# Kernel optimization log

Hardware: AMD Instinct MI355X
Metric: run time of the kernel (lower is better)

The kernel has to match this reference:

```python
import jax, jax.numpy as jnp
import numpy as np

DEPTH, HEADS, DIM, DIM_HEAD, MLP = 2, 8, 512, 64, 2048
INNER = HEADS * DIM_HEAD  # == DIM here, but project_out is still True since dim_head != dim
NEG = -1e9


def _ln(t, g, b):
    mu = t.mean(-1, keepdims=True)
    var = ((t - mu) ** 2).mean(-1, keepdims=True)
    return (t - mu) / jnp.sqrt(var + 1e-5) * g + b


def _heads(t):
    b, n, hd = t.shape
    return t.reshape(b, n, HEADS, hd // HEADS).transpose(0, 2, 1, 3)  # b h n d


def _merge(t):
    b, h, n, d = t.shape
    return t.transpose(0, 2, 1, 3).reshape(b, n, h * d)


def kat_forward(x, kx, rd, clst, mask, kmask,
                ln1_g, ln1_b, Wqkv, Wout, bout, ln2_g, ln2_b, W1, b1, W2, b2):
    scale = DIM_HEAD ** -0.5
    # att_mask[b,1,n,m]: True where attention is disallowed (mask_i * kmask_j < 0.5)
    att_mask = (jnp.einsum('bid,bjd->bij', mask, kmask) < 0.5)[:, None]
    krd = rd[:, None]                      # [b,1,m,n]
    krdT = jnp.swapaxes(krd, -1, -2)       # [b,1,n,m]
    keep = (kmask >= 0.5)                  # kernel_mask fill-with-0 complement
    k_reps, atten = [], []
    for l in range(DEPTH):
        # pre-norm applied in-place before residual (as in the original)
        xn = _ln(x, ln1_g[l], ln1_b[l])
        kxn = _ln(kx, ln1_g[l], ln1_b[l])
        cn = _ln(clst, ln1_g[l], ln1_b[l])

        def qkv(t):
            q, k, v = jnp.split(t @ Wqkv[l], 3, axis=-1)
            return _heads(q), _heads(k), _heads(v)

        tq, tk, tv = qkv(xn)
        kq, kk, kv = qkv(kxn)
        cq, _, _ = qkv(cn)

        # patch -> kernel attention, krd-weighted dual softmax
        dots = jnp.einsum('bhid,bhjd->bhij', tq, kk) * scale      # [b,h,n,m]
        dots = jnp.where(att_mask, NEG, dots)
        attn_t = jax.nn.softmax(dots * 24, -1) * krdT             # temperature branch (attention map out)
        attn = jax.nn.softmax(dots, -1) * krdT
        x_ = _merge(jnp.einsum('bhij,bhjd->bhid', attn, kv)) @ Wout[l] + bout[l]

        # kernel -> patch attention
        kd = jnp.einsum('bhid,bhjd->bhij', kq, tk) * scale        # [b,h,m,n]
        kd = jnp.where(jnp.swapaxes(att_mask, -1, -2), NEG, kd)
        kattn = jax.nn.softmax(kd, -1) * krd
        kx_ = _merge(jnp.einsum('bhij,bhjd->bhid', kattn, tv)) @ Wout[l] + bout[l]

        # class token -> kernel attention
        cd = jnp.einsum('bhid,bhjd->bhij', cq, kk) * scale        # [b,h,1,m]
        cd = jnp.where(att_mask[:, :, :1], NEG, cd)
        c_ = _merge(jnp.einsum('bhij,bhjd->bhid', jax.nn.softmax(cd, -1), kv)) @ Wout[l] + bout[l]

        x, kx, clst = xn + x_, kxn + kx_, cn + c_

        def ff(t):
            tn = _ln(t, ln2_g[l], ln2_b[l])
            return jax.nn.gelu(tn @ W1[l] + b1[l], approximate=False) @ W2[l] + b2[l]

        x, kx, clst = ff(x) + x, ff(kx) + kx, ff(clst) + clst
        k_reps.append(kx * keep)
        atten.append(jnp.swapaxes(attn_t, -1, -2))  # [b,h,m,n]
    return jnp.stack(k_reps), clst, jnp.stack(atten)


def setup_inputs() -> dict:
    key = jax.random.key(0)
    ks = jax.random.split(key, 16)
    b, n, m = 4, 2048, 256
    s = 0.02
    L = DEPTH
    return {
        'x': jax.random.normal(ks[0], (b, n, DIM), jnp.float32),
        'kx': jax.random.normal(ks[1], (b, m, DIM), jnp.float32),
        'rd': jax.random.uniform(ks[2], (b, m, n), jnp.float32),
        'clst': jax.random.normal(ks[3], (b, 1, DIM), jnp.float32),
        'mask': jnp.ones((b, n, 1), jnp.float32),
        'kmask': jax.random.uniform(ks[4], (b, m, 1), jnp.float32),
        'ln1_g': jnp.ones((L, DIM), jnp.float32),
        'ln1_b': jnp.zeros((L, DIM), jnp.float32),
        'Wqkv': s * jax.random.normal(ks[5], (L, DIM, 3 * INNER), jnp.float32),
        'Wout': s * jax.random.normal(ks[6], (L, INNER, DIM), jnp.float32),
        'bout': jnp.zeros((L, DIM), jnp.float32),
        'ln2_g': jnp.ones((L, DIM), jnp.float32),
        'ln2_b': jnp.zeros((L, DIM), jnp.float32),
        'W1': s * jax.random.normal(ks[7], (L, DIM, MLP), jnp.float32),
        'b1': jnp.zeros((L, MLP), jnp.float32),
        'W2': s * jax.random.normal(ks[8], (L, MLP, DIM), jnp.float32),
        'b2': jnp.zeros((L, DIM), jnp.float32),
    }


def reference(x, kx, rd, clst, mask, kmask, ln1_g, ln1_b, Wqkv, Wout, bout,
              ln2_g, ln2_b, W1, b1, W2, b2):
    return kat_forward(x, kx, rd, clst, mask, kmask, ln1_g, ln1_b, Wqkv, Wout,
                       bout, ln2_g, ln2_b, W1, b1, W2, b2)
```

## Files before the change

### kernel.cpp

```cpp
#include <hip/hip_runtime.h>
#include <hip/hip_bf16.h>
#include <cstddef>

#define DEV __device__ __forceinline__

constexpr int Bb  = 4;
constexpr int Nn  = 2048;
constexpr int MK  = 256;
constexpr int Dd  = 512;
constexpr int Hh  = 8;
constexpr int DH  = 64;
constexpr int QLD = 1536;
constexpr int MLPD = 2048;
constexpr int NTOK = Bb * Nn + Bb * MK + Bb;
constexpr int KXOFF = Bb * Nn;
constexpr int CLOFF = Bb * Nn + Bb * MK;
constexpr float SCALE = 0.125f;
constexpr float NEGV  = -1e9f;

typedef __attribute__((ext_vector_type(8))) short short8;
typedef __attribute__((ext_vector_type(4))) float f32x4;

DEV float4 ldf4(const float* p) { return *reinterpret_cast<const float4*>(p); }

DEV void gload16(const short* g, short* l) {
  __builtin_amdgcn_global_load_lds(
      (const __attribute__((address_space(1))) void*)g,
      (__attribute__((address_space(3))) void*)l, 16, 0, 0);
}

DEV float waveMax(float v) {
#pragma unroll
  for (int o = 32; o; o >>= 1) v = fmaxf(v, __shfl_xor(v, o));
  return v;
}
DEV float waveSum(float v) {
#pragma unroll
  for (int o = 32; o; o >>= 1) v += __shfl_xor(v, o);
  return v;
}
DEV float blockMax256(float v, float* red) {
  v = waveMax(v);
  __syncthreads();
  if ((threadIdx.x & 63) == 0) red[threadIdx.x >> 6] = v;
  __syncthreads();
  return fmaxf(fmaxf(red[0], red[1]), fmaxf(red[2], red[3]));
}
DEV float blockSum256(float v, float* red) {
  v = waveSum(v);
  __syncthreads();
  if ((threadIdx.x & 63) == 0) red[threadIdx.x >> 6] = v;
  __syncthreads();
  return red[0] + red[1] + red[2] + red[3];
}
DEV float gelu_f(float x) { return 0.5f * x * (1.f + erff(x * 0.70710678118654752f)); }
DEV float pow24(float e1) {
  float e2 = e1 * e1, e4 = e2 * e2, e8 = e4 * e4, e16 = e8 * e8;
  return e16 * e8;
}

__global__ __launch_bounds__(256)
void copy3_kernel(const float* __restrict__ x, const float* __restrict__ kx,
                  const float* __restrict__ c, float* __restrict__ dst) {
  const int idx = blockIdx.x * 256 + threadIdx.x;
  const int row = idx >> 7;
  float4 v;
  if (row < KXOFF) v = ldf4(x + (size_t)idx * 4);
  else if (row < CLOFF) v = ldf4(kx + (size_t)idx * 4 - (size_t)KXOFF * Dd);
  else v = ldf4(c + (size_t)idx * 4 - (size_t)CLOFF * Dd);
  *reinterpret_cast<float4*>(dst + (size_t)idx * 4) = v;
}

__global__ __launch_bounds__(64)
void ln_kernel(const float* __restrict__ in, const float* __restrict__ gw,
               const float* __restrict__ bw, float* __restrict__ out,
               __hip_bfloat16* __restrict__ outb) {
  const int row = blockIdx.x;
  const int t = threadIdx.x;
  const float* p = in + (size_t)row * Dd + t * 8;
  float4 v0 = ldf4(p), v1 = ldf4(p + 4);
  float s = v0.x + v0.y + v0.z + v0.w + v1.x + v1.y + v1.z + v1.w;
  float q = v0.x*v0.x + v0.y*v0.y + v0.z*v0.z + v0.w*v0.w
          + v1.x*v1.x + v1.y*v1.y + v1.z*v1.z + v1.w*v1.w;
  s = waveSum(s); q = waveSum(q);
  const float mu = s * (1.f / Dd);
  const float rstd = rsqrtf(fmaxf(q * (1.f / Dd) - mu * mu, 0.f) + 1e-5f);
  float4 g0 = ldf4(gw + t * 8), g1 = ldf4(gw + t * 8 + 4);
  float4 b0 = ldf4(bw + t * 8), b1 = ldf4(bw + t * 8 + 4);
  float o[8];
  o[0] = (v0.x - mu) * rstd * g0.x + b0.x;
  o[1] = (v0.y - mu) * rstd * g0.y + b0.y;
  o[2] = (v0.z - mu) * rstd * g0.z + b0.z;
  o[3] = (v0.w - mu) * rstd * g0.w + b0.w;
  o[4] = (v1.x - mu) * rstd * g1.x + b1.x;
  o[5] = (v1.y - mu) * rstd * g1.y + b1.y;
  o[6] = (v1.z - mu) * rstd * g1.z + b1.z;
  o[7] = (v1.w - mu) * rstd * g1.w + b1.w;
  float* op = out + (size_t)row * Dd + t * 8;
  *reinterpret_cast<float4*>(op)     = make_float4(o[0], o[1], o[2], o[3]);
  *reinterpret_cast<float4*>(op + 4) = make_float4(o[4], o[5], o[6], o[7]);
  __hip_bfloat16* ob = outb + (size_t)row * Dd + t * 8;
#pragma unroll
  for (int e = 0; e < 8; ++e) ob[e] = __float2bfloat16(o[e]);
}

struct GArgs {
  const short* A;  long asb; int lda;
  const short* Bt; long bsb; int ldb;
  float* C; __hip_bfloat16* Cb;
  long czo, czi; int ldc;
  const float* bias;
  const float* res; int ldr;
  int M, N, K;
};

template<int BM, int BN, int EPI>
__global__ __launch_bounds__(256)
void mgemm(GArgs g) {
  constexpr int WMW = (BN >= 128) ? 2 : 4;
  constexpr int WNW = 4 / WMW;
  constexpr int WM = BM / WMW, WN = BN / WNW;
  constexpr int FM = WM / 16, FN = WN / 16;
  __shared__ __align__(16) short As[BM * 64];
  __shared__ __align__(16) short Bs[BN * 64];
  const int tid = threadIdx.x, l = tid & 63, w = tid >> 6;
  const int wm = (WNW == 2) ? (w >> 1) : w;
  const int wn = (WNW == 2) ? (w & 1) : 0;
  int bx = blockIdx.x, by = blockIdx.y;
  {
    const int gx = gridDim.x, nwg = gx * gridDim.y;
    const int orig = by * gx + bx;
    const int xcd = orig & 7, pos = orig >> 3;
    const int q = nwg >> 3, rmd = nwg & 7;
    const int s = (xcd < rmd ? xcd * (q + 1) : rmd * (q + 1) + (xcd - rmd) * q) + pos;
    bx = s % gx; by = s / gx;
  }
  const int z = blockIdx.z;
  const short* Ab = g.A + (size_t)z * g.asb;
  const short* Bb_ = g.Bt + (size_t)z * g.bsb;
  f32x4 acc[FM][FN] = {};
  const int lr = l & 15, lg = l >> 4;

  for (int k0 = 0; k0 < g.K; k0 += 64) {
    __syncthreads();
#pragma unroll
    for (int it = 0; it < BM / 32; ++it) {
      int idx = tid + it * 256, r = idx >> 3, c = idx & 7;
      int gm = by * BM + r;
      if (gm >= g.M) gm = g.M - 1;
      gload16(Ab + (size_t)gm * g.lda + k0 + ((c ^ (r & 7)) * 8), As + idx * 8);
    }
#pragma unroll
    for (int it = 0; it < BN / 32; ++it) {
      int idx = tid + it * 256, r = idx >> 3, c = idx & 7;
      int gn = bx * BN + r;
      gload16(Bb_ + (size_t)gn * g.ldb + k0 + ((c ^ (r & 7)) * 8), Bs + idx * 8);
    }
    __syncthreads();
#pragma unroll
    for (int ks = 0; ks < 2; ++ks) {
      short8 a[FM], b[FN];
#pragma unroll
      for (int fm = 0; fm < FM; ++fm) {
        int rr = wm * WM + fm * 16 + lr;
        int ch = (ks * 4 + lg) ^ (rr & 7);
        a[fm] = *reinterpret_cast<const short8*>(As + rr * 64 + ch * 8);
      }
#pragma unroll
      for (int fn = 0; fn < FN; ++fn) {
        int rn = wn * WN + fn * 16 + lr;
        int ch = (ks * 4 + lg) ^ (rn & 7);
        b[fn] = *reinterpret_cast<const short8*>(Bs + rn * 64 + ch * 8);
      }
#pragma unroll
      for (int fm = 0; fm < FM; ++fm)
#pragma unroll
        for (int fn = 0; fn < FN; ++fn)
          acc[fm][fn] = __builtin_amdgcn_mfma_f32_16x16x32_bf16(a[fm], b[fn], acc[fm][fn], 0, 0, 0);
    }
  }

  const size_t zoff = (size_t)(z >> 3) * g.czo + (size_t)(z & 7) * g.czi;
#pragma unroll
  for (int fm = 0; fm < FM; ++fm) {
#pragma unroll
    for (int fn = 0; fn < FN; ++fn) {
#pragma unroll
      for (int r = 0; r < 4; ++r) {
        int m = by * BM + wm * WM + fm * 16 + lg * 4 + r;
        int n = bx * BN + wn * WN + fn * 16 + lr;
        if (m >= g.M) continue;
        float v = acc[fm][fn][r];
        size_t coff = zoff + (size_t)m * g.ldc + n;
        if (EPI == 0) {
          g.C[coff] = v;
        } else if (EPI == 2) {
          v += g.bias[n] + g.res[(size_t)m * g.ldr + n];
          g.C[coff] = v;
        } else if (EPI == 3) {
          v = gelu_f(v + g.bias[n]);
          g.Cb[coff] = __float2bfloat16(v);
        } else {
          g.Cb[coff] = __float2bfloat16(v);
        }
      }
    }
  }
}

template<int BM, int BN, int EPI>
static void launch_mgemm(const GArgs& g, int zdim, hipStream_t s) {
  dim3 grid((g.N + BN - 1) / BN, (g.M + BM - 1) / BM, zdim);
  mgemm<BM, BN, EPI><<<grid, 256, 0, s>>>(g);
}

__global__ __launch_bounds__(512)
void score_sx_kernel(const short* __restrict__ Q, const short* __restrict__ Km,
                     const float* __restrict__ mask, const float* __restrict__ kmask,
                     const float* __restrict__ rdT,
                     __hip_bfloat16* __restrict__ P1, __hip_bfloat16* __restrict__ E24) {
  __shared__ __align__(16) short As[128 * 64];
  __shared__ __align__(16) short Bs[256 * 64];
  __shared__ float red[128 * 2];
  __shared__ float red2[128 * 4];
  const int tid = threadIdx.x, l = tid & 63, w = tid >> 6;
  const int wm = w >> 1, wn = w & 1;
  const int by = blockIdx.x, bh = blockIdx.y;
  const int b = bh >> 3;
  const short* Ab = Q + (size_t)bh * Nn * 128;
  const short* Bb = Km + (size_t)bh * MK * 128;
  const int lr = l & 15, lg = l >> 4;
  f32x4 acc[2][8] = {};

  for (int k0 = 0; k0 < 128; k0 += 64) {
    __syncthreads();
#pragma unroll
    for (int it = 0; it < 2; ++it) {
      int idx = tid + it * 512, r = idx >> 3, c = idx & 7;
      gload16(Ab + (size_t)(by * 128 + r) * 128 + k0 + ((c ^ (r & 7)) * 8), As + idx * 8);
    }
#pragma unroll
    for (int it = 0; it < 4; ++it) {
      int idx = tid + it * 512, r = idx >> 3, c = idx & 7;
      gload16(Bb + (size_t)r * 128 + k0 + ((c ^ (r & 7)) * 8), Bs + idx * 8);
    }
    __syncthreads();
#pragma unroll
    for (int ks = 0; ks < 2; ++ks) {
      short8 a[2], bv[8];
#pragma unroll
      for (int fm = 0; fm < 2; ++fm) {
        int rr = wm * 32 + fm * 16 + lr;
        int ch = (ks * 4 + lg) ^ (rr & 7);
        a[fm] = *reinterpret_cast<const short8*>(As + rr * 64 + ch * 8);
      }
#pragma unroll
      for (int fn = 0; fn < 8; ++fn) {
        int rn = wn * 128 + fn * 16 + lr;
        int ch = (ks * 4 + lg) ^ (rn & 7);
        bv[fn] = *reinterpret_cast<const short8*>(Bs + rn * 64 + ch * 8);
      }
#pragma unroll
      for (int fm = 0; fm < 2; ++fm)
#pragma unroll
        for (int fn = 0; fn < 8; ++fn)
          acc[fm][fn] = __builtin_amdgcn_mfma_f32_16x16x32_bf16(a[fm], bv[fn], acc[fm][fn], 0, 0, 0);
    }
  }
  {
    float colm[8];
#pragma unroll
    for (int fn = 0; fn < 8; ++fn)
      colm[fn] = kmask[b * MK + wn * 128 + fn * 16 + lr];
#pragma unroll
    for (int fm = 0; fm < 2; ++fm)
#pragma unroll
      for (int r = 0; r < 4; ++r) {
        float rm = mask[(size_t)b * Nn + by * 128 + wm * 32 + fm * 16 + lg * 4 + r];
#pragma unroll
        for (int fn = 0; fn < 8; ++fn)
          acc[fm][fn][r] = (rm * colm[fn] < 0.5f) ? NEGV : acc[fm][fn][r] * SCALE;
      }
  }
  float mx[2][4];
#pragma unroll
  for (int fm = 0; fm < 2; ++fm)
#pragma unroll
    for (int r = 0; r < 4; ++r) {
      float m = -3.4e38f;
#pragma unroll
      for (int fn = 0; fn < 8; ++fn) m = fmaxf(m, acc[fm][fn][r]);
#pragma unroll
      for (int o = 8; o; o >>= 1) m = fmaxf(m, __shfl_xor(m, o));
      mx[fm][r] = m;
    }
  __syncthreads();
  if (lr == 0) {
#pragma unroll
    for (int fm = 0; fm < 2; ++fm)
#pragma unroll
      for (int r = 0; r < 4; ++r)
        red[(wm * 32 + fm * 16 + lg * 4 + r) * 2 + wn] = mx[fm][r];
  }
  __syncthreads();
#pragma unroll
  for (int fm = 0; fm < 2; ++fm)
#pragma unroll
    for (int r = 0; r < 4; ++r) {
      int row = wm * 32 + fm * 16 + lg * 4 + r;
      mx[fm][r] = fmaxf(red[row * 2], red[row * 2 + 1]);
    }
  float s1[2][4], s24[2][4];
#pragma unroll
  for (int fm = 0; fm < 2; ++fm)
#pragma unroll
    for (int r = 0; r < 4; ++r) {
      float a1 = 0.f, a24 = 0.f;
#pragma unroll
      for (int fn = 0; fn < 8; ++fn) {
        float e1 = __expf(acc[fm][fn][r] - mx[fm][r]);
        acc[fm][fn][r] = e1;
        a1 += e1;
        a24 += pow24(e1);
      }
#pragma unroll
      for (int o = 8; o; o >>= 1) { a1 += __shfl_xor(a1, o); a24 += __shfl_xor(a24, o); }
      s1[fm][r] = a1; s24[fm][r] = a24;
    }
  __syncthreads();
  if (lr == 0) {
#pragma unroll
    for (int fm = 0; fm < 2; ++fm)
#pragma unroll
      for (int r = 0; r < 4; ++r) {
        int row = wm * 32 + fm * 16 + lg * 4 + r;
        red2[row * 4 + wn * 2]     = s1[fm][r];
        red2[row * 4 + wn * 2 + 1] = s24[fm][r];
      }
  }
  __syncthreads();
#pragma unroll
  for (int fm = 0; fm < 2; ++fm)
#pragma unroll
    for (int r = 0; r < 4; ++r) {
      int row = wm * 32 + fm * 16 + lg * 4 + r;
      s1[fm][r]  = 1.f / (red2[row * 4] + red2[row * 4 + 2]);
      s24[fm][r] = 1.f / (red2[row * 4 + 1] + red2[row * 4 + 3]);
    }
#pragma unroll
  for (int fm = 0; fm < 2; ++fm) {
#pragma unroll
    for (int r = 0; r < 4; ++r) {
      int m = by * 128 + wm * 32 + fm * 16 + lg * 4 + r;
      const float* rp = rdT + ((size_t)b * Nn + m) * MK;
      size_t obase = ((size_t)bh * Nn + m) * MK;
#pragma unroll
      for (int fn = 0; fn < 8; ++fn) {
        int n = wn * 128 + fn * 16 + lr;
        float e1 = acc[fm][fn][r];
        float rv = rp[n];
        P1[obase + n]  = __float2bfloat16(e1 * s1[fm][r] * rv);
        E24[obase + n] = __float2bfloat16(pow24(e1) * s24[fm][r] * rv);
      }
    }
  }
}

__global__ __launch_bounds__(256)
void score_sk_kernel(const short* __restrict__ Qk, const short* __restrict__ Kt,
                     const float* __restrict__ mask, const float* __restrict__ kmask,
                     const float* __restrict__ rd, __hip_bfloat16* __restrict__ P2) {
  __shared__ __align__(16) short As[16 * 64];
  __shared__ __align__(16) short Bs[256 * 64];
  __shared__ float redm[16 * 4];
  __shared__ float reds[16 * 4];
  const int tid = threadIdx.x, l = tid & 63, w = tid >> 6;
  const int lr = l & 15, lg = l >> 4;
  const int bh = blockIdx.x, j0 = blockIdx.y * 16, b = bh >> 3;
  const short* Ab = Qk + ((size_t)bh * MK + j0) * 64;
  const short* Bb = Kt + (size_t)bh * Nn * 64;
  f32x4 acc[32];
#pragma unroll
  for (int q = 0; q < 32; ++q) acc[q] = f32x4{0.f, 0.f, 0.f, 0.f};
  if (tid < 128) {
    int r = tid >> 3, c = tid & 7;
    gload16(Ab + (size_t)r * 64 + ((c ^ (r & 7)) * 8), As + tid * 8);
  }
#pragma unroll
  for (int nc = 0; nc < 8; ++nc) {
    __syncthreads();
#pragma unroll
    for (int it = 0; it < 8; ++it) {
      int idx = tid + it * 256, r = idx >> 3, c = idx & 7;
      gload16(Bb + (size_t)(nc * 256 + r) * 64 + ((c ^ (r & 7)) * 8), Bs + idx * 8);
    }
    __syncthreads();
#pragma unroll
    for (int ks = 0; ks < 2; ++ks) {
      short8 a;
      {
        int ch = (ks * 4 + lg) ^ (lr & 7);
        a = *reinterpret_cast<const short8*>(As + lr * 64 + ch * 8);
      }
#pragma unroll
      for (int fn = 0; fn < 4; ++fn) {
        int rn = w * 64 + fn * 16 + lr;
        int ch = (ks * 4 + lg) ^ (rn & 7);
        short8 bv = *reinterpret_cast<const short8*>(Bs + rn * 64 + ch * 8);
        acc[nc * 4 + fn] =
            __builtin_amdgcn_mfma_f32_16x16x32_bf16(a, bv, acc[nc * 4 + fn], 0, 0, 0);
      }
    }
  }
  float rm[4];
#pragma unroll
  for (int rr = 0; rr < 4; ++rr) rm[rr] = kmask[b * MK + j0 + lg * 4 + rr];
  float mx[4] = {-3.4e38f, -3.4e38f, -3.4e38f, -3.4e38f};
#pragma unroll
  for (int q = 0; q < 32; ++q) {
    int n = (q >> 2) * 256 + w * 64 + (q & 3) * 16 + lr;
    float cm = mask[(size_t)b * Nn + n];
#pragma unroll
    for (int rr = 0; rr < 4; ++rr) {
      float v = (rm[rr] * cm < 0.5f) ? NEGV : acc[q][rr] * SCALE;
      acc[q][rr] = v;
      mx[rr] = fmaxf(mx[rr], v);
    }
  }
#pragma unroll
  for (int o = 8; o; o >>= 1)
#pragma unroll
    for (int rr = 0; rr < 4; ++rr) mx[rr] = fmaxf(mx[rr], __shfl_xor(mx[rr], o));
  __syncthreads();
  if (lr == 0) {
#pragma unroll
    for (int rr = 0; rr < 4; ++rr) redm[(lg * 4 + rr) * 4 + w] = mx[rr];
  }
  __syncthreads();
#pragma unroll
  for (int rr = 0; rr < 4; ++rr) {
    int row = lg * 4 + rr;
    mx[rr] = fmaxf(fmaxf(redm[row * 4], redm[row * 4 + 1]),
                   fmaxf(redm[row * 4 + 2], redm[row * 4 + 3]));
  }
  float sm[4] = {0.f, 0.f, 0.f, 0.f};
#pragma unroll
  for (int q = 0; q < 32; ++q)
#pragma unroll
    for (int rr = 0; rr < 4; ++rr) {
      float e = __expf(acc[q][rr] - mx[rr]);
      acc[q][rr] = e;
      sm[rr] += e;
    }
#pragma unroll
  for (int o = 8; o; o >>= 1)
#pragma unroll
    for (int rr = 0; rr < 4; ++rr) sm[rr] += __shfl_xor(sm[rr], o);
  __syncthreads();
  if (lr == 0) {
#pragma unroll
    for (int rr = 0; rr < 4; ++rr) reds[(lg * 4 + rr) * 4 + w] = sm[rr];
  }
  __syncthreads();
  float inv[4];
#pragma unroll
  for (int rr = 0; rr < 4; ++rr) {
    int row = lg * 4 + rr;
    inv[rr] = 1.f / (reds[row * 4] + reds[row * 4 + 1] + reds[row * 4 + 2] + reds[row * 4 + 3]);
  }
#pragma unroll
  for (int rr = 0; rr < 4; ++rr) {
    int j = j0 + lg * 4 + rr;
    const float* rp = rd + (size_t)(b * MK + j) * Nn;
    __hip_bfloat16* pp = P2 + ((size_t)bh * MK + j) * Nn;
#pragma unroll
    for (int q = 0; q < 32; ++q) {
      int n = (q >> 2) * 256 + w * 64 + (q & 3) * 16 + lr;
      pp[n] = __float2bfloat16(acc[q][rr] * inv[rr] * rp[n]);
    }
  }
}

__global__ __launch_bounds__(256)
void at_tr_kernel(const __hip_bfloat16* __restrict__ E, float* __restrict__ atten) {
  __shared__ __hip_bfloat16 t[64][72];
  const int bh = blockIdx.x;
  const int i0 = blockIdx.y * 64, j0 = blockIdx.z * 64;
  const int tid = threadIdx.x;
#pragma unroll
  for (int it = 0; it < 2; ++it) {
    int idx = tid + it * 256, r = idx >> 3, c8 = (idx & 7) * 8;
    short8 v = *reinterpret_cast<const short8*>(
        (const short*)E + ((size_t)bh * Nn + i0 + r) * MK + j0 + c8);
#pragma unroll
    for (int e = 0; e < 8; ++e)
      *reinterpret_cast<short*>(&t[r][c8 + e]) = v[e];
  }
  __syncthreads();
#pragma unroll
  for (int it = 0; it < 4; ++it) {
    int idx = tid + it * 256, jr = idx >> 4, c4 = (idx & 15) * 4;
    float4 o;
    o.x = __bfloat162float(t[c4 + 0][jr]);
    o.y = __bfloat162float(t[c4 + 1][jr]);
    o.z = __bfloat162float(t[c4 + 2][jr]);
    o.w = __bfloat162float(t[c4 + 3][jr]);
    *reinterpret_cast<float4*>(
        atten + ((size_t)bh * MK + j0 + jr) * Nn + i0 + c4) = o;
  }
}

__global__ __launch_bounds__(256)
void rd_tr_kernel(const float* __restrict__ rd, float* __restrict__ rdT) {
  __shared__ float tb[64][65];
  const int b = blockIdx.x;
  const int i0 = blockIdx.y * 64, j0 = blockIdx.z * 64;
  const int tid = threadIdx.x;
#pragma unroll
  for (int it = 0; it < 4; ++it) {
    int idx = tid + it * 256, r = idx >> 4, c4 = (idx & 15) * 4;
    float4 v = ldf4(rd + ((size_t)(b * MK + j0 + r)) * Nn + i0 + c4);
    tb[r][c4 + 0] = v.x; tb[r][c4 + 1] = v.y; tb[r][c4 + 2] = v.z; tb[r][c4 + 3] = v.w;
  }
  __syncthreads();
#pragma unroll
  for (int it = 0; it < 4; ++it) {
    int idx = tid + it * 256, r = idx >> 4, c4 = (idx & 15) * 4;
    float4 o = make_float4(tb[c4 + 0][r], tb[c4 + 1][r], tb[c4 + 2][r], tb[c4 + 3][r]);
    *reinterpret_cast<float4*>(rdT + ((size_t)(b * Nn + i0 + r)) * MK + j0 + c4) = o;
  }
}

struct WtArgs {
  const float* W[8];
  __hip_bfloat16* T[8];
  int K[8], N[8];
};
__global__ __launch_bounds__(256)
void wtrans_all_kernel(WtArgs a) {
  __shared__ float t[64][65];
  const int e = blockIdx.z;
  const int K = a.K[e], N = a.N[e];
  const int n0 = blockIdx.x * 64, k0 = blockIdx.y * 64;
  if (n0 >= N || k0 >= K) return;
  const float* W = a.W[e];
  __hip_bfloat16* WT = a.T[e];
  const int tid = threadIdx.x;
#pragma unroll
  for (int it = 0; it < 4; ++it) {
    int idx = tid + it * 256, r = idx >> 4, f = idx & 15;
    float4 v = ldf4(W + (size_t)(k0 + r) * N + n0 + f * 4);
    t[r][f * 4 + 0] = v.x; t[r][f * 4 + 1] = v.y;
    t[r][f * 4 + 2] = v.z; t[r][f * 4 + 3] = v.w;
  }
  __syncthreads();
#pragma unroll
  for (int it = 0; it < 4; ++it) {
    int idx = tid + it * 256, r = idx >> 4, c4 = (idx & 15) * 4;
    __hip_bfloat16* op = WT + (size_t)(n0 + r) * K + k0 + c4;
#pragma unroll
    for (int e2 = 0; e2 < 4; ++e2) op[e2] = __float2bfloat16(t[c4 + e2][r]);
  }
}

template<bool Q_SPLIT>
__global__ __launch_bounds__(256)
void split_kernel(const float* __restrict__ qkv, __hip_bfloat16* __restrict__ qout,
                  __hip_bfloat16* __restrict__ kout, int T) {
  const int idx = blockIdx.x * 256 + threadIdx.x;
  const int token = idx >> 7, c8 = (idx & 127) * 8;
  const int b = token / T, i = token - b * T;
  const float* p = qkv + (size_t)token * QLD + c8;
  float v[8];
  float4 a = ldf4(p), c = ldf4(p + 4);
  v[0]=a.x; v[1]=a.y; v[2]=a.z; v[3]=a.w; v[4]=c.x; v[5]=c.y; v[6]=c.z; v[7]=c.w;
  if (c8 < 512) {
    int h = c8 >> 6, d = c8 & 63;
    if (Q_SPLIT) {
      __hip_bfloat16* q = qout + ((size_t)((b * 8 + h) * T + i)) * 128 + d;
#pragma unroll
      for (int e = 0; e < 8; ++e) {
        __hip_bfloat16 hi = __float2bfloat16(v[e]);
        q[e] = hi;
        q[64 + e] = __float2bfloat16(v[e] - __bfloat162float(hi));
      }
    } else {
      __hip_bfloat16* q = qout + ((size_t)((b * 8 + h) * T + i)) * 64 + d;
#pragma unroll
      for (int e = 0; e < 8; ++e) q[e] = __float2bfloat16(v[e]);
    }
  } else {
    int cc = c8 - 512, h = cc >> 6, d = cc & 63;
    if (Q_SPLIT) {
      __hip_bfloat16* k = kout + ((size_t)((b * 8 + h) * T + i)) * 64 + d;
#pragma unroll
      for (int e = 0; e < 8; ++e) k[e] = __float2bfloat16(v[e]);
    } else {
      __hip_bfloat16* k = kout + ((size_t)((b * 8 + h) * T + i)) * 128 + d;
#pragma unroll
      for (int e = 0; e < 8; ++e) {
        __hip_bfloat16 hi = __float2bfloat16(v[e]);
        k[e] = hi;
        k[64 + e] = __float2bfloat16(v[e] - __bfloat162float(hi));
      }
    }
  }
}

__global__ __launch_bounds__(256)
void vtrans_kernel(const float* __restrict__ qkv, __hip_bfloat16* __restrict__ vT, int T) {
  __shared__ float t[64][65];
  const int bh = blockIdx.x, b = bh >> 3, h = bh & 7;
  const int i0 = blockIdx.y * 64;
  const int tid = threadIdx.x;
#pragma unroll
  for (int it = 0; it < 4; ++it) {
    int idx = tid + it * 256, r = idx >> 4, f = idx & 15;
    float4 v = ldf4(qkv + (size_t)(b * T + i0 + r) * QLD + 2 * Dd + h * 64 + f * 4);
    t[r][f * 4 + 0] = v.x; t[r][f * 4 + 1] = v.y;
    t[r][f * 4 + 2] = v.z; t[r][f * 4 + 3] = v.w;
  }
  __syncthreads();
#pragma unroll
  for (int it = 0; it < 4; ++it) {
    int idx = tid + it * 256, d = idx >> 4, c4 = (idx & 15) * 4;
    __hip_bfloat16* op = vT + (size_t)(bh * 64 + d) * T + i0 + c4;
#pragma unroll
    for (int e = 0; e < 4; ++e) op[e] = __float2bfloat16(t[c4 + e][d]);
  }
}

__global__ __launch_bounds__(256)
void attn_c_kernel(const float* __restrict__ cqkv, const float* __restrict__ kqkv,
                   const float* __restrict__ mask, const float* __restrict__ kmask,
                   __hip_bfloat16* __restrict__ c_pre) {
  __shared__ __align__(16) float kv_s[MK][DH];
  __shared__ __align__(16) float q_s[DH];
  __shared__ float pbuf[MK];
  __shared__ float red8[8];
  __shared__ float redpv[4][DH];
  const int tid = threadIdx.x;
  const int bh = blockIdx.x, b = bh >> 3, h = bh & 7;
  const float* vp = kqkv + ((size_t)(b * MK + tid)) * QLD + 2 * Dd + h * DH;
#pragma unroll
  for (int q4 = 0; q4 < 16; ++q4)
    *reinterpret_cast<float4*>(&kv_s[tid][q4 * 4]) = ldf4(vp + q4 * 4);
  if (tid < DH) q_s[tid] = cqkv[(size_t)b * QLD + h * DH + tid];
  __syncthreads();
  const float* kp = kqkv + ((size_t)(b * MK + tid)) * QLD + Dd + h * DH;
  float dot = 0.f;
#pragma unroll
  for (int q4 = 0; q4 < 16; ++q4) {
    float4 kv4 = ldf4(kp + q4 * 4);
    float4 qv = ldf4(&q_s[q4 * 4]);
    dot = fmaf(qv.x, kv4.x, dot);
    dot = fmaf(qv.y, kv4.y, dot);
    dot = fmaf(qv.z, kv4.z, dot);
    dot = fmaf(qv.w, kv4.w, dot);
  }
  const float dm = (mask[(size_t)b * Nn] * kmask[b * MK + tid] < 0.5f) ? NEGV : dot * SCALE;
  const float mx = blockMax256(dm, red8);
  const float e = __expf(dm - mx);
  const float s = blockSum256(e, red8);
  pbuf[tid] = e / s;
  __syncthreads();
  const int d = tid & 63, g = tid >> 6;
  float acc = 0.f;
#pragma unroll 8
  for (int jj = 0; jj < 64; ++jj)
    acc = fmaf(pbuf[g * 64 + jj], kv_s[g * 64 + jj][d], acc);
  redpv[g][d] = acc;
  __syncthreads();
  if (tid < DH)
    c_pre[(size_t)b * Dd + h * DH + tid] = __float2bfloat16(
        redpv[0][tid] + redpv[1][tid] + redpv[2][tid] + redpv[3][tid]);
}

__global__ void kreps_kernel(const float* __restrict__ kx, const float* __restrict__ kmask,
                             float* __restrict__ o) {
  const int idx = blockIdx.x * 256 + threadIdx.x;
  const int bj = idx >> 9;
  const float keep = (kmask[bj] >= 0.5f) ? 1.f : 0.f;
  o[idx] = kx[idx] * keep;
}
__global__ void cout_kernel(const float* __restrict__ c_s, float* __restrict__ o) {
  const int idx = blockIdx.x * 256 + threadIdx.x;
  o[idx] = c_s[idx];
}

static GArgs ga_base() { GArgs g = {}; return g; }

extern "C" void kernel_launch(void* const* d_in, const int* in_sizes, int n_in,
                              void* d_out, int out_size, void* d_ws, size_t ws_size,
                              hipStream_t stream) {
  (void)in_sizes; (void)n_in; (void)out_size; (void)ws_size;
  const float* x_in  = (const float*)d_in[0];
  const float* kx_in = (const float*)d_in[1];
  const float* rd    = (const float*)d_in[2];
  const float* c_in  = (const float*)d_in[3];
  const float* mask  = (const float*)d_in[4];
  const float* kmask = (const float*)d_in[5];
  const float* ln1g  = (const float*)d_in[6];
  const float* ln1b  = (const float*)d_in[7];
  const float* Wqkv  = (const float*)d_in[8];
  const float* Woutw = (const float*)d_in[9];
  const float* boutw = (const float*)d_in[10];
  const float* ln2g  = (const float*)d_in[11];
  const float* ln2b  = (const float*)d_in[12];
  const float* W1    = (const float*)d_in[13];
  const float* b1    = (const float*)d_in[14];
  const float* W2    = (const float*)d_in[15];
  const float* b2    = (const float*)d_in[16];
  float* out = (float*)d_out;

  float* ws = (float*)d_ws;
  size_t off = 0;
  auto alloc = [&](size_t n) { float* p = ws + off; off += (n + 15) & ~(size_t)15; return p; };
  float* xcat_s    = alloc((size_t)NTOK * Dd);
  float* xcat_n    = alloc((size_t)NTOK * Dd);
  float* xcat_nb_f = alloc((size_t)NTOK * Dd / 2);
  float* pre_cat_f = alloc((size_t)NTOK * Dd / 2);
  float* qkv       = alloc((size_t)NTOK * QLD);
  float* P1_f      = alloc((size_t)32 * Nn * MK / 2);
  float* E24_f     = alloc((size_t)32 * Nn * MK / 2);
  float* P2_f      = alloc((size_t)32 * MK * Nn / 2);
  float* tq_s_f    = alloc((size_t)32 * Nn * 128 / 2);
  float* kk_s_f    = alloc((size_t)32 * MK * 128 / 2);
  float* tk_hi_f   = alloc((size_t)32 * Nn * 64 / 2);
  float* kq_hi_f   = alloc((size_t)32 * MK * 64 / 2);
  float* tvT_f     = alloc((size_t)32 * 64 * Nn / 2);
  float* kvT_f     = alloc((size_t)32 * 64 * MK / 2);
  float* rdT       = alloc((size_t)Bb * Nn * MK);
  float* WqkvT_f   = alloc((size_t)2 * QLD * Dd / 2);
  float* WoutT_f   = alloc((size_t)2 * Dd * Dd / 2);
  float* W1T_f     = alloc((size_t)2 * MLPD * Dd / 2);
  float* W2T_f     = alloc((size_t)2 * Dd * MLPD / 2);

  __hip_bfloat16* xcat_nb = (__hip_bfloat16*)xcat_nb_f;
  __hip_bfloat16* pre_cat = (__hip_bfloat16*)pre_cat_f;
  __hip_bfloat16* P1b     = (__hip_bfloat16*)P1_f;
  __hip_bfloat16* E24b    = (__hip_bfloat16*)E24_f;
  __hip_bfloat16* P2b     = (__hip_bfloat16*)P2_f;
  __hip_bfloat16* tq_s    = (__hip_bfloat16*)tq_s_f;
  __hip_bfloat16* kk_s    = (__hip_bfloat16*)kk_s_f;
  __hip_bfloat16* tk_hi   = (__hip_bfloat16*)tk_hi_f;
  __hip_bfloat16* kq_hi   = (__hip_bfloat16*)kq_hi_f;
  __hip_bfloat16* tvT     = (__hip_bfloat16*)tvT_f;
  __hip_bfloat16* kvT     = (__hip_bfloat16*)kvT_f;
  __hip_bfloat16* WqkvT   = (__hip_bfloat16*)WqkvT_f;
  __hip_bfloat16* WoutT   = (__hip_bfloat16*)WoutT_f;
  __hip_bfloat16* W1T     = (__hip_bfloat16*)W1T_f;
  __hip_bfloat16* W2T     = (__hip_bfloat16*)W2T_f;
  __hip_bfloat16* hid     = (__hip_bfloat16*)qkv;

  const size_t CL_OFF = (size_t)2 * Bb * MK * Dd;
  const size_t AT_OFF = CL_OFF + (size_t)Bb * Dd;

  copy3_kernel<<<(NTOK * 128) / 256, 256, 0, stream>>>(x_in, kx_in, c_in, xcat_s);
  rd_tr_kernel<<<dim3(Bb, Nn / 64, MK / 64), 256, 0, stream>>>(rd, rdT);
  {
    WtArgs a;
    for (int l = 0; l < 2; ++l) {
      a.W[l * 4 + 0] = Wqkv + (size_t)l * Dd * QLD;  a.T[l * 4 + 0] = WqkvT + (size_t)l * QLD * Dd;
      a.K[l * 4 + 0] = Dd;   a.N[l * 4 + 0] = QLD;
      a.W[l * 4 + 1] = Woutw + (size_t)l * Dd * Dd;  a.T[l * 4 + 1] = WoutT + (size_t)l * Dd * Dd;
      a.K[l * 4 + 1] = Dd;   a.N[l * 4 + 1] = Dd;
      a.W[l * 4 + 2] = W1 + (size_t)l * Dd * MLPD;   a.T[l * 4 + 2] = W1T + (size_t)l * MLPD * Dd;
      a.K[l * 4 + 2] = Dd;   a.N[l * 4 + 2] = MLPD;
      a.W[l * 4 + 3] = W2 + (size_t)l * MLPD * Dd;   a.T[l * 4 + 3] = W2T + (size_t)l * Dd * MLPD;
      a.K[l * 4 + 3] = MLPD; a.N[l * 4 + 3] = Dd;
    }
    wtrans_all_kernel<<<dim3(32, 32, 8), 256, 0, stream>>>(a);
  }

  for (int l = 0; l < 2; ++l) {
    const float* bo  = boutw + (size_t)l * Dd;
    const float* b1l = b1 + (size_t)l * MLPD;
    const float* b2l = b2 + (size_t)l * Dd;
    __hip_bfloat16* WqkvTl = WqkvT + (size_t)l * QLD * Dd;
    __hip_bfloat16* WoutTl = WoutT + (size_t)l * Dd * Dd;
    __hip_bfloat16* W1Tl   = W1T + (size_t)l * MLPD * Dd;
    __hip_bfloat16* W2Tl   = W2T + (size_t)l * Dd * MLPD;

    ln_kernel<<<NTOK, 64, 0, stream>>>(xcat_s, ln1g + l * Dd, ln1b + l * Dd, xcat_n, xcat_nb);

    {
      GArgs g = ga_base();
      g.A = (const short*)xcat_nb; g.lda = Dd;
      g.Bt = (const short*)WqkvTl; g.ldb = Dd;
      g.C = qkv; g.ldc = QLD;
      g.M = NTOK; g.N = QLD; g.K = Dd;
      launch_mgemm<128, 128, 0>(g, 1, stream);
    }

    split_kernel<true><<<(Bb * Nn * 128) / 256, 256, 0, stream>>>(qkv, tq_s, tk_hi, Nn);
    split_kernel<false><<<(Bb * MK * 128) / 256, 256, 0, stream>>>(
        qkv + (size_t)KXOFF * QLD, kq_hi, kk_s, MK);
    vtrans_kernel<<<dim3(32, Nn / 64), 256, 0, stream>>>(qkv, tvT, Nn);
    vtrans_kernel<<<dim3(32, MK / 64), 256, 0, stream>>>(qkv + (size_t)KXOFF * QLD, kvT, MK);

    attn_c_kernel<<<Bb * Hh, 256, 0, stream>>>(qkv + (size_t)CLOFF * QLD,
                                               qkv + (size_t)KXOFF * QLD, mask, kmask,
                                               pre_cat + (size_t)CLOFF * Dd);

    score_sx_kernel<<<dim3(Nn / 128, 32), 512, 0, stream>>>(
        (const short*)tq_s, (const short*)kk_s, mask, kmask, rdT, P1b, E24b);
    at_tr_kernel<<<dim3(32, Nn / 64, MK / 64), 256, 0, stream>>>(
        E24b, out + AT_OFF + (size_t)l * 32 * MK * Nn);
    {
      GArgs g = ga_base();
      g.A = (const short*)P1b; g.asb = (long)Nn * MK; g.lda = MK;
      g.Bt = (const short*)kvT; g.bsb = (long)64 * MK; g.ldb = MK;
      g.Cb = pre_cat; g.czo = (long)Nn * Dd; g.czi = 64; g.ldc = Dd;
      g.M = Nn; g.N = 64; g.K = MK;
      launch_mgemm<128, 64, 4>(g, 32, stream);
    }
    score_sk_kernel<<<dim3(32, MK / 16), 256, 0, stream>>>(
        (const short*)kq_hi, (const short*)tk_hi, mask, kmask, rd, P2b);
    {
      GArgs g = ga_base();
      g.A = (const short*)P2b; g.asb = (long)MK * Nn; g.lda = Nn;
      g.Bt = (const short*)tvT; g.bsb = (long)64 * Nn; g.ldb = Nn;
      g.Cb = pre_cat + (size_t)KXOFF * Dd; g.czo = (long)MK * Dd; g.czi = 64; g.ldc = Dd;
      g.M = MK; g.N = 64; g.K = Nn;
      launch_mgemm<64, 64, 4>(g, 32, stream);
    }

    {
      GArgs g = ga_base();
      g.A = (const short*)pre_cat; g.lda = Dd;
      g.Bt = (const short*)WoutTl; g.ldb = Dd;
      g.C = xcat_s; g.ldc = Dd; g.bias = bo; g.res = xcat_n; g.ldr = Dd;
      g.M = NTOK; g.N = Dd; g.K = Dd;
      launch_mgemm<128, 64, 2>(g, 1, stream);
    }

    ln_kernel<<<NTOK, 64, 0, stream>>>(xcat_s, ln2g + l * Dd, ln2b + l * Dd, xcat_n, xcat_nb);
    {
      GArgs g = ga_base();
      g.A = (const short*)xcat_nb; g.lda = Dd;
      g.Bt = (const short*)W1Tl; g.ldb = Dd;
      g.Cb = hid; g.ldc = MLPD; g.bias = b1l;
      g.M = NTOK; g.N = MLPD; g.K = Dd;
      launch_mgemm<128, 128, 3>(g, 1, stream);
      GArgs h = ga_base();
      h.A = (const short*)hid; h.lda = MLPD;
      h.Bt = (const short*)W2Tl; h.ldb = MLPD;
      h.C = xcat_s; h.ldc = Dd; h.bias = b2l; h.res = xcat_s; h.ldr = Dd;
      h.M = NTOK; h.N = Dd; h.K = MLPD;
      launch_mgemm<128, 64, 2>(h, 1, stream);
    }

    kreps_kernel<<<(Bb * MK * Dd) / 256, 256, 0, stream>>>(
        xcat_s + (size_t)KXOFF * Dd, kmask, out + (size_t)l * Bb * MK * Dd);
  }
  cout_kernel<<<(Bb * Dd) / 256, 256, 0, stream>>>(xcat_s + (size_t)CLOFF * Dd, out + CL_OFF);
}
```

Measured before the change: 772.3 us.

## Fuse QKV split/transpose kernels, drop fp32 LN output, loop at_tr over j

Merges the two split kernels and two V-transpose kernels into one prep_attn launch. LayerNorm no longer writes an fp32 copy; the out-projection residual now reads the bf16 normalized activations via a new epilogue. at_tr_kernel processes all four j-tiles per block instead of one block per tile. The aim is fewer launches and less fp32 memory traffic, at the cost of lower residual precision (bf16 instead of fp32) and fewer, larger transpose blocks.

```diff
diff --git a/kernel.cpp b/kernel.cpp
--- a/kernel.cpp
+++ b/kernel.cpp
@@ -73,8 +73,7 @@
 
 __global__ __launch_bounds__(64)
 void ln_kernel(const float* __restrict__ in, const float* __restrict__ gw,
-               const float* __restrict__ bw, float* __restrict__ out,
-               __hip_bfloat16* __restrict__ outb) {
+               const float* __restrict__ bw, __hip_bfloat16* __restrict__ outb) {
   const int row = blockIdx.x;
   const int t = threadIdx.x;
   const float* p = in + (size_t)row * Dd + t * 8;
@@ -96,9 +95,6 @@
   o[5] = (v1.y - mu) * rstd * g1.y + b1.y;
   o[6] = (v1.z - mu) * rstd * g1.z + b1.z;
   o[7] = (v1.w - mu) * rstd * g1.w + b1.w;
-  float* op = out + (size_t)row * Dd + t * 8;
-  *reinterpret_cast<float4*>(op)     = make_float4(o[0], o[1], o[2], o[3]);
-  *reinterpret_cast<float4*>(op + 4) = make_float4(o[4], o[5], o[6], o[7]);
   __hip_bfloat16* ob = outb + (size_t)row * Dd + t * 8;
 #pragma unroll
   for (int e = 0; e < 8; ++e) ob[e] = __float2bfloat16(o[e]);
@@ -110,7 +106,7 @@
   float* C; __hip_bfloat16* Cb;
   long czo, czi; int ldc;
   const float* bias;
-  const float* res; int ldr;
+  const float* res; const __hip_bfloat16* resb; int ldr;
   int M, N, K;
 };
 
@@ -197,6 +193,9 @@
         } else if (EPI == 2) {
           v += g.bias[n] + g.res[(size_t)m * g.ldr + n];
           g.C[coff] = v;
+        } else if (EPI == 5) {
+          v += g.bias[n] + __bfloat162float(g.resb[(size_t)m * g.ldr + n]);
+          g.C[coff] = v;
         } else if (EPI == 3) {
           v = gelu_f(v + g.bias[n]);
           g.Cb[coff] = __float2bfloat16(v);
@@ -212,6 +211,82 @@
 static void launch_mgemm(const GArgs& g, int zdim, hipStream_t s) {
   dim3 grid((g.N + BN - 1) / BN, (g.M + BM - 1) / BM, zdim);
   mgemm<BM, BN, EPI><<<grid, 256, 0, s>>>(g);
+}
+
+__global__ __launch_bounds__(256)
+void prep_attn_kernel(const float* __restrict__ qkv_x, const float* __restrict__ qkv_k,
+                      __hip_bfloat16* __restrict__ tq_s, __hip_bfloat16* __restrict__ tk_hi,
+                      __hip_bfloat16* __restrict__ kq_hi, __hip_bfloat16* __restrict__ kk_s,
+                      __hip_bfloat16* __restrict__ tvT, __hip_bfloat16* __restrict__ kvT) {
+  __shared__ float t[64][65];
+  const int blk = blockIdx.x, tid = threadIdx.x;
+  if (blk < 4096 + 512) {
+    const bool isX = blk < 4096;
+    const int T = isX ? Nn : MK;
+    const float* qkv = isX ? qkv_x : qkv_k;
+    const int idx = (isX ? blk : blk - 4096) * 256 + tid;
+    const int token = idx >> 7, c8 = (idx & 127) * 8;
+    const int b = token / T, i = token - b * T;
+    const float* p = qkv + (size_t)token * QLD + c8;
+    float v[8];
+    float4 a = ldf4(p), c = ldf4(p + 4);
+    v[0]=a.x; v[1]=a.y; v[2]=a.z; v[3]=a.w; v[4]=c.x; v[5]=c.y; v[6]=c.z; v[7]=c.w;
+    if (c8 < 512) {
+      int h = c8 >> 6, d = c8 & 63;
+      if (isX) {
+        __hip_bfloat16* q = tq_s + ((size_t)((b * 8 + h) * T + i)) * 128 + d;
+#pragma unroll
+        for (int e = 0; e < 8; ++e) {
+          __hip_bfloat16 hi = __float2bfloat16(v[e]);
+          q[e] = hi;
+          q[64 + e] = __float2bfloat16(v[e] - __bfloat162float(hi));
+        }
+      } else {
+        __hip_bfloat16* q = kq_hi + ((size_t)((b * 8 + h) * T + i)) * 64 + d;
+#pragma unroll
+        for (int e = 0; e < 8; ++e) q[e] = __float2bfloat16(v[e]);
+      }
+    } else {
+      int cc = c8 - 512, h = cc >> 6, d = cc & 63;
+      if (isX) {
+        __hip_bfloat16* k = tk_hi + ((size_t)((b * 8 + h) * T + i)) * 64 + d;
+#pragma unroll
+        for (int e = 0; e < 8; ++e) k[e] = __float2bfloat16(v[e]);
+      } else {
+        __hip_bfloat16* k = kk_s + ((size_t)((b * 8 + h) * T + i)) * 128 + d;
+#pragma unroll
+        for (int e = 0; e < 8; ++e) {
+          __hip_bfloat16 hi = __float2bfloat16(v[e]);
+          k[e] = hi;
+          k[64 + e] = __float2bfloat16(v[e] - __bfloat162float(hi));
+        }
+      }
+    }
+    return;
+  }
+  const bool isX = blk < 5632;
+  const int r = isX ? blk - 4608 : blk - 5632;
+  const int T = isX ? Nn : MK;
+  const int tilesPerBh = T / 64;
+  const int bh = r / tilesPerBh, i0 = (r % tilesPerBh) * 64;
+  const int b = bh >> 3, h = bh & 7;
+  const float* qkv = isX ? qkv_x : qkv_k;
+  __hip_bfloat16* vT = isX ? tvT : kvT;
+#pragma unroll
+  for (int it = 0; it < 4; ++it) {
+    int idx = tid + it * 256, rr = idx >> 4, f = idx & 15;
+    float4 v = ldf4(qkv + (size_t)(b * T + i0 + rr) * QLD + 2 * Dd + h * 64 + f * 4);
+    t[rr][f * 4 + 0] = v.x; t[rr][f * 4 + 1] = v.y;
+    t[rr][f * 4 + 2] = v.z; t[rr][f * 4 + 3] = v.w;
+  }
+  __syncthreads();
+#pragma unroll
+  for (int it = 0; it < 4; ++it) {
+    int idx = tid + it * 256, d = idx >> 4, c4 = (idx & 15) * 4;
+    __hip_bfloat16* op = vT + (size_t)(bh * 64 + d) * T + i0 + c4;
+#pragma unroll
+    for (int e = 0; e < 4; ++e) op[e] = __float2bfloat16(t[c4 + e][d]);
+  }
 }
 
 __global__ __launch_bounds__(512)
@@ -485,28 +560,32 @@
 void at_tr_kernel(const __hip_bfloat16* __restrict__ E, float* __restrict__ atten) {
   __shared__ __hip_bfloat16 t[64][72];
   const int bh = blockIdx.x;
-  const int i0 = blockIdx.y * 64, j0 = blockIdx.z * 64;
+  const int i0 = blockIdx.y * 64;
   const int tid = threadIdx.x;
-#pragma unroll
-  for (int it = 0; it < 2; ++it) {
-    int idx = tid + it * 256, r = idx >> 3, c8 = (idx & 7) * 8;
-    short8 v = *reinterpret_cast<const short8*>(
-        (const short*)E + ((size_t)bh * Nn + i0 + r) * MK + j0 + c8);
-#pragma unroll
-    for (int e = 0; e < 8; ++e)
-      *reinterpret_cast<short*>(&t[r][c8 + e]) = v[e];
-  }
-  __syncthreads();
-#pragma unroll
-  for (int it = 0; it < 4; ++it) {
-    int idx = tid + it * 256, jr = idx >> 4, c4 = (idx & 15) * 4;
-    float4 o;
-    o.x = __bfloat162float(t[c4 + 0][jr]);
-    o.y = __bfloat162float(t[c4 + 1][jr]);
-    o.z = __bfloat162float(t[c4 + 2][jr]);
-    o.w = __bfloat162float(t[c4 + 3][jr]);
-    *reinterpret_cast<float4*>(
-        atten + ((size_t)bh * MK + j0 + jr) * Nn + i0 + c4) = o;
+  for (int jt = 0; jt < 4; ++jt) {
+    const int j0 = jt * 64;
+    if (jt) __syncthreads();
+#pragma unroll
+    for (int it = 0; it < 2; ++it) {
+      int idx = tid + it * 256, r = idx >> 3, c8 = (idx & 7) * 8;
+      short8 v = *reinterpret_cast<const short8*>(
+          (const short*)E + ((size_t)bh * Nn + i0 + r) * MK + j0 + c8);
+#pragma unroll
+      for (int e = 0; e < 8; ++e)
+        *reinterpret_cast<short*>(&t[r][c8 + e]) = v[e];
+    }
+    __syncthreads();
+#pragma unroll
+    for (int it = 0; it < 4; ++it) {
+      int idx = tid + it * 256, jr = idx >> 4, c4 = (idx & 15) * 4;
+      float4 o;
+      o.x = __bfloat162float(t[c4 + 0][jr]);
+      o.y = __bfloat162float(t[c4 + 1][jr]);
+      o.z = __bfloat162float(t[c4 + 2][jr]);
+      o.w = __bfloat162float(t[c4 + 3][jr]);
+      *reinterpret_cast<float4*>(
+          atten + ((size_t)bh * MK + j0 + jr) * Nn + i0 + c4) = o;
+    }
   }
 }
 
@@ -560,73 +639,6 @@
     __hip_bfloat16* op = WT + (size_t)(n0 + r) * K + k0 + c4;
 #pragma unroll
     for (int e2 = 0; e2 < 4; ++e2) op[e2] = __float2bfloat16(t[c4 + e2][r]);
-  }
-}
-
-template<bool Q_SPLIT>
-__global__ __launch_bounds__(256)
-void split_kernel(const float* __restrict__ qkv, __hip_bfloat16* __restrict__ qout,
-                  __hip_bfloat16* __restrict__ kout, int T) {
-  const int idx = blockIdx.x * 256 + threadIdx.x;
-  const int token = idx >> 7, c8 = (idx & 127) * 8;
-  const int b = token / T, i = token - b * T;
-  const float* p = qkv + (size_t)token * QLD + c8;
-  float v[8];
-  float4 a = ldf4(p), c = ldf4(p + 4);
-  v[0]=a.x; v[1]=a.y; v[2]=a.z; v[3]=a.w; v[4]=c.x; v[5]=c.y; v[6]=c.z; v[7]=c.w;
-  if (c8 < 512) {
-    int h = c8 >> 6, d = c8 & 63;
-    if (Q_SPLIT) {
-      __hip_bfloat16* q = qout + ((size_t)((b * 8 + h) * T + i)) * 128 + d;
-#pragma unroll
-      for (int e = 0; e < 8; ++e) {
-        __hip_bfloat16 hi = __float2bfloat16(v[e]);
-        q[e] = hi;
-        q[64 + e] = __float2bfloat16(v[e] - __bfloat162float(hi));
-      }
-    } else {
-      __hip_bfloat16* q = qout + ((size_t)((b * 8 + h) * T + i)) * 64 + d;
-#pragma unroll
-      for (int e = 0; e < 8; ++e) q[e] = __float2bfloat16(v[e]);
-    }
-  } else {
-    int cc = c8 - 512, h = cc >> 6, d = cc & 63;
-    if (Q_SPLIT) {
-      __hip_bfloat16* k = kout + ((size_t)((b * 8 + h) * T + i)) * 64 + d;
-#pragma unroll
-      for (int e = 0; e < 8; ++e) k[e] = __float2bfloat16(v[e]);
-    } else {
-      __hip_bfloat16* k = kout + ((size_t)((b * 8 + h) * T + i)) * 128 + d;
-#pragma unroll
-      for (int e = 0; e < 8; ++e) {
-        __hip_bfloat16 hi = __float2bfloat16(v[e]);
-        k[e] = hi;
-        k[64 + e] = __float2bfloat16(v[e] - __bfloat162float(hi));
-      }
-    }
-  }
-}
-
-__global__ __launch_bounds__(256)
-void vtrans_kernel(const float* __restrict__ qkv, __hip_bfloat16* __restrict__ vT, int T) {
-  __shared__ float t[64][65];
-  const int bh = blockIdx.x, b = bh >> 3, h = bh & 7;
-  const int i0 = blockIdx.y * 64;
-  const int tid = threadIdx.x;
-#pragma unroll
-  for (int it = 0; it < 4; ++it) {
-    int idx = tid + it * 256, r = idx >> 4, f = idx & 15;
-    float4 v = ldf4(qkv + (size_t)(b * T + i0 + r) * QLD + 2 * Dd + h * 64 + f * 4);
-    t[r][f * 4 + 0] = v.x; t[r][f * 4 + 1] = v.y;
-    t[r][f * 4 + 2] = v.z; t[r][f * 4 + 3] = v.w;
-  }
-  __syncthreads();
-#pragma unroll
-  for (int it = 0; it < 4; ++it) {
-    int idx = tid + it * 256, d = idx >> 4, c4 = (idx & 15) * 4;
-    __hip_bfloat16* op = vT + (size_t)(bh * 64 + d) * T + i0 + c4;
-#pragma unroll
-    for (int e = 0; e < 4; ++e) op[e] = __float2bfloat16(t[c4 + e][d]);
   }
 }
 
@@ -717,7 +729,6 @@
   size_t off = 0;
   auto alloc = [&](size_t n) { float* p = ws + off; off += (n + 15) & ~(size_t)15; return p; };
   float* xcat_s    = alloc((size_t)NTOK * Dd);
-  float* xcat_n    = alloc((size_t)NTOK * Dd);
   float* xcat_nb_f = alloc((size_t)NTOK * Dd / 2);
   float* pre_cat_f = alloc((size_t)NTOK * Dd / 2);
   float* qkv       = alloc((size_t)NTOK * QLD);
@@ -782,7 +793,7 @@
     __hip_bfloat16* W1Tl   = W1T + (size_t)l * MLPD * Dd;
     __hip_bfloat16* W2Tl   = W2T + (size_t)l * Dd * MLPD;
 
-    ln_kernel<<<NTOK, 64, 0, stream>>>(xcat_s, ln1g + l * Dd, ln1b + l * Dd, xcat_n, xcat_nb);
+    ln_kernel<<<NTOK, 64, 0, stream>>>(xcat_s, ln1g + l * Dd, ln1b + l * Dd, xcat_nb);
 
     {
       GArgs g = ga_base();
@@ -793,11 +804,8 @@
       launch_mgemm<128, 128, 0>(g, 1, stream);
     }
 
-    split_kernel<true><<<(Bb * Nn * 128) / 256, 256, 0, stream>>>(qkv, tq_s, tk_hi, Nn);
-    split_kernel<false><<<(Bb * MK * 128) / 256, 256, 0, stream>>>(
-        qkv + (size_t)KXOFF * QLD, kq_hi, kk_s, MK);
-    vtrans_kernel<<<dim3(32, Nn / 64), 256, 0, stream>>>(qkv, tvT, Nn);
-    vtrans_kernel<<<dim3(32, MK / 64), 256, 0, stream>>>(qkv + (size_t)KXOFF * QLD, kvT, MK);
+    prep_attn_kernel<<<5760, 256, 0, stream>>>(
+        qkv, qkv + (size_t)KXOFF * QLD, tq_s, tk_hi, kq_hi, kk_s, tvT, kvT);
 
     attn_c_kernel<<<Bb * Hh, 256, 0, stream>>>(qkv + (size_t)CLOFF * QLD,
                                                qkv + (size_t)KXOFF * QLD, mask, kmask,
@@ -805,7 +813,7 @@
 
     score_sx_kernel<<<dim3(Nn / 128, 32), 512, 0, stream>>>(
         (const short*)tq_s, (const short*)kk_s, mask, kmask, rdT, P1b, E24b);
-    at_tr_kernel<<<dim3(32, Nn / 64, MK / 64), 256, 0, stream>>>(
+    at_tr_kernel<<<dim3(32, Nn / 64), 256, 0, stream>>>(
         E24b, out + AT_OFF + (size_t)l * 32 * MK * Nn);
     {
       GArgs g = ga_base();
@@ -830,12 +838,12 @@
       GArgs g = ga_base();
       g.A = (const short*)pre_cat; g.lda = Dd;
       g.Bt = (const short*)WoutTl; g.ldb = Dd;
-      g.C = xcat_s; g.ldc = Dd; g.bias = bo; g.res = xcat_n; g.ldr = Dd;
+      g.C = xcat_s; g.ldc = Dd; g.bias = bo; g.resb = xcat_nb; g.ldr = Dd;
       g.M = NTOK; g.N = Dd; g.K = Dd;
-      launch_mgemm<128, 64, 2>(g, 1, stream);
-    }
-
-    ln_kernel<<<NTOK, 64, 0, stream>>>(xcat_s, ln2g + l * Dd, ln2b + l * Dd, xcat_n, xcat_nb);
+      launch_mgemm<128, 64, 5>(g, 1, stream);
+    }
+
+    ln_kernel<<<NTOK, 64, 0, stream>>>(xcat_s, ln2g + l * Dd, ln2b + l * Dd, xcat_nb);
     {
       GArgs g = ga_base();
       g.A = (const short*)xcat_nb; g.lda = Dd;
```

Measured after the change: 732.6 us. -5.1%, faster.
